# Kernel optimization log

Measured on AMD Instinct MI355X. Metric: run time of the kernel, lower is better.

## Reference

```python
import jax, jax.numpy as jnp
import numpy as np
import math

B, S, DIM = 2, 2048, 1024
N_HEADS, N_KV = 16, 4
HD = DIM // N_HEADS          # 64
N_REP = N_HEADS // N_KV      # 4
ROPE_THETA = 5000.0


def _rope_tables(seqlen, head_dim, theta):
    freqs = 1.0 / (theta ** (np.arange(0, head_dim, 2, dtype=np.float32) / head_dim))
    angles = np.outer(np.arange(seqlen, dtype=np.float32), freqs)  # [S, HD/2]
    return jnp.asarray(np.cos(angles)), jnp.asarray(np.sin(angles))


def setup_inputs() -> dict:
    key = jax.random.key(0)
    ks = jax.random.split(key, 6)
    x = jax.random.normal(ks[0], (B, S, DIM), dtype=jnp.float32)
    cos, sin = _rope_tables(S, HD, ROPE_THETA)
    # additive causal mask: 0 on/below diagonal, -inf above
    mask = jnp.where(jnp.tril(jnp.ones((S, S), dtype=bool)), 0.0, -jnp.inf).astype(jnp.float32)
    wq = jax.random.normal(ks[1], (DIM, N_HEADS * HD), dtype=jnp.float32) * 0.02
    wk = jax.random.normal(ks[2], (DIM, N_KV * HD), dtype=jnp.float32) * 0.02
    wv = jax.random.normal(ks[3], (DIM, N_KV * HD), dtype=jnp.float32) * 0.02
    wo = jax.random.normal(ks[4], (N_HEADS * HD, DIM), dtype=jnp.float32) * 0.02
    return {"x": x, "cos": cos, "sin": sin, "mask": mask,
            "wq": wq, "wk": wk, "wv": wv, "wo": wo}


def _apply_rope(t, cos, sin):
    # t: [B, S, H, HD]; even/odd interleaved pairs form complex numbers
    te, to = t[..., 0::2], t[..., 1::2]               # [B,S,H,HD/2]
    c = cos[None, :, None, :]
    s = sin[None, :, None, :]
    re = te * c - to * s
    im = te * s + to * c
    return jnp.stack([re, im], axis=-1).reshape(t.shape)  # re-interleave


def reference(x, cos, sin, mask, wq, wk, wv, wo):
    bsz, seqlen, _ = x.shape
    q = (x @ wq).reshape(bsz, seqlen, N_HEADS, HD)
    k = (x @ wk).reshape(bsz, seqlen, N_KV, HD)
    v = (x @ wv).reshape(bsz, seqlen, N_KV, HD)
    q = _apply_rope(q, cos, sin)
    k = _apply_rope(k, cos, sin)
    # GQA: group query heads as [kv_head g, rep r] instead of repeating K/V
    qg = q.reshape(bsz, seqlen, N_KV, N_REP, HD)
    scores = jnp.einsum('bsgrd,btgd->bgrst', qg, k) / math.sqrt(HD)  # [B,G,R,S,S]
    scores = scores + mask[None, None, None, :, :]
    p = jax.nn.softmax(scores, axis=-1)
    out = jnp.einsum('bgrst,btgd->bsgrd', p, v)       # [B,S,G,R,HD]
    out = out.reshape(bsz, seqlen, N_HEADS * HD)
    return out @ wo
```

## Files before the change

### kernel.cpp

```cpp
#include <hip/hip_runtime.h>
#include <math.h>

#define S_LEN 2048
#define B_SZ 2

typedef __bf16 bf16_8 __attribute__((ext_vector_type(8)));
typedef float  f32_4  __attribute__((ext_vector_type(4)));

__device__ __forceinline__ unsigned short ftob(float f) {
  union { __bf16 h; unsigned short u; } cv;
  cv.h = (__bf16)f;
  return cv.u;
}

__device__ __forceinline__ void gll16(const unsigned short* g, unsigned short* l) {
  __builtin_amdgcn_global_load_lds(
      (const __attribute__((address_space(1))) unsigned int*)g,
      (__attribute__((address_space(3))) unsigned int*)l, 16, 0, 0);
}

#define QSCALE (0.125f * 1.44269504f)

__device__ __forceinline__ void tr_tile(const float* __restrict__ W,
                                        unsigned short* __restrict__ Wt,
                                        int N, int bx, int by, float (*T)[33])
{
  const int k0 = by * 32, n0 = bx * 32;
  const int r = threadIdx.x >> 3, c4 = (threadIdx.x & 7) * 4;
  const float4 v = *(const float4*)&W[(size_t)(k0 + r) * N + n0 + c4];
  T[r][c4 + 0] = v.x; T[r][c4 + 1] = v.y;
  T[r][c4 + 2] = v.z; T[r][c4 + 3] = v.w;
  __syncthreads();
  ushort4 o;
  o.x = ftob(T[c4 + 0][r]); o.y = ftob(T[c4 + 1][r]);
  o.z = ftob(T[c4 + 2][r]); o.w = ftob(T[c4 + 3][r]);
  *(ushort4*)&Wt[(size_t)(n0 + r) * 1024 + k0 + c4] = o;
}

__global__ __launch_bounds__(256) void prep1(
    const float* __restrict__ x, const float* __restrict__ wq,
    const float* __restrict__ wk, const float* __restrict__ wv,
    unsigned short* __restrict__ xb, unsigned short* __restrict__ wqkvt)
{
  __shared__ float T[32][33];
  const int idx = blockIdx.x;
  if (idx < 1024) {
    tr_tile(wq, wqkvt, 1024, idx & 31, idx >> 5, T);
  } else if (idx < 1280) {
    const int i = idx - 1024;
    tr_tile(wk, wqkvt + 1024 * 1024, 256, i & 7, i >> 3, T);
  } else if (idx < 1536) {
    const int i = idx - 1280;
    tr_tile(wv, wqkvt + 1280 * 1024, 256, i & 7, i >> 3, T);
  } else {
    const int i = idx - 1536;
#pragma unroll
    for (int j = 0; j < 4; ++j) {
      const int id = i * 1024 + (int)threadIdx.x + j * 256;
      const float4 v = ((const float4*)x)[id];
      ushort4 o;
      o.x = ftob(v.x); o.y = ftob(v.y); o.z = ftob(v.z); o.w = ftob(v.w);
      ((ushort4*)xb)[id] = o;
    }
  }
}

__global__ __launch_bounds__(256) void prep2(
    const float* __restrict__ wo, unsigned short* __restrict__ wot)
{
  __shared__ float T[32][33];
  tr_tile(wo, wot, 1024, blockIdx.x & 31, blockIdx.x >> 5, T);
}

__global__ __launch_bounds__(256) void gemm_qkv(
    const unsigned short* __restrict__ A, const unsigned short* __restrict__ Bt,
    unsigned short* __restrict__ qb, unsigned short* __restrict__ Kimg,
    unsigned short* __restrict__ Vimg,
    const float* __restrict__ cosT, const float* __restrict__ sinT)
{
  __shared__ unsigned short sm[9216];
  unsigned short* As = sm;
  unsigned short* Bs = sm + 2048;
  const int bm = blockIdx.y * 64, bn0 = blockIdx.x;
  const int tid = threadIdx.x;
  const int w = tid >> 6, lane = tid & 63, l16 = lane & 15, quad = lane >> 4;
  const int mh = (w & 1) * 32, nh = (w >> 1) * 64;

  f32_4 acc[2][4];
#pragma unroll
  for (int mt = 0; mt < 2; ++mt)
#pragma unroll
    for (int nt = 0; nt < 4; ++nt) acc[mt][nt] = (f32_4){0.f, 0.f, 0.f, 0.f};

  for (int k0 = 0; k0 < 1024; k0 += 32) {
    __syncthreads();
    gll16(&A[(size_t)(bm + (tid >> 2)) * 1024 + k0 + (tid & 3) * 8], &As[tid * 8]);
    gll16(&Bt[(size_t)(bn0 * 128 + (tid >> 2)) * 1024 + k0 + (tid & 3) * 8], &Bs[tid * 8]);
    {
      const int cb = tid + 256;
      gll16(&Bt[(size_t)(bn0 * 128 + (cb >> 2)) * 1024 + k0 + (cb & 3) * 8], &Bs[cb * 8]);
    }
    __syncthreads();
    bf16_8 af[2], bf[4];
#pragma unroll
    for (int mt = 0; mt < 2; ++mt)
      af[mt] = *(const bf16_8*)&As[(mh + mt * 16 + l16) * 32 + quad * 8];
#pragma unroll
    for (int nt = 0; nt < 4; ++nt)
      bf[nt] = *(const bf16_8*)&Bs[(nh + nt * 16 + l16) * 32 + quad * 8];
#pragma unroll
    for (int mt = 0; mt < 2; ++mt)
#pragma unroll
      for (int nt = 0; nt < 4; ++nt)
        acc[mt][nt] = __builtin_amdgcn_mfma_f32_16x16x32_bf16(af[mt], bf[nt], acc[mt][nt], 0, 0, 0);
  }

  const int colbase = bn0 * 128;
  if (colbase < 1024) {
#pragma unroll
    for (int mt = 0; mt < 2; ++mt)
#pragma unroll
      for (int r = 0; r < 4; ++r) {
        const int row = bm + mh + mt * 16 + quad * 4 + r;
        const int s = row & (S_LEN - 1);
#pragma unroll
        for (int nt = 0; nt < 4; ++nt) {
          const int col = colbase + nh + nt * 16 + l16;
          float val = acc[mt][nt][r];
          const float pv = __shfl_xor(val, 1);
          const int fi = (col & 63) >> 1;
          const float cc = cosT[s * 32 + fi], ss = sinT[s * 32 + fi];
          val = (l16 & 1) ? fmaf(pv, ss, val * cc) : fmaf(val, cc, -(pv * ss));
          qb[(size_t)row * 1024 + col] = ftob(val * QSCALE);
        }
      }
  } else if (colbase < 1280) {
#pragma unroll
    for (int mt = 0; mt < 2; ++mt)
#pragma unroll
      for (int r = 0; r < 4; ++r) {
        const int row = bm + mh + mt * 16 + quad * 4 + r;
        const int s = row & (S_LEN - 1), bi = row >> 11;
        const int tile = s >> 6, key = s & 63;
#pragma unroll
        for (int nt = 0; nt < 4; ++nt) {
          const int col = colbase + nh + nt * 16 + l16;
          float val = acc[mt][nt][r];
          const float pv = __shfl_xor(val, 1);
          const int fi = (col & 63) >> 1;
          const float cc = cosT[s * 32 + fi], ss = sinT[s * 32 + fi];
          val = (l16 & 1) ? fmaf(pv, ss, val * cc) : fmaf(val, cc, -(pv * ss));
          const int gcol = col - 1024, g = gcol >> 6, d = gcol & 63;
          Kimg[(size_t)((bi * 4 + g) * 32 + tile) * 4608 + key * 72 + d] = ftob(val);
        }
      }
  } else {
    __syncthreads();
    const int half = nh >> 6;
    unsigned short* Ts = sm + half * 4608;
#pragma unroll
    for (int mt = 0; mt < 2; ++mt)
#pragma unroll
      for (int r = 0; r < 4; ++r) {
        const int key = mh + mt * 16 + quad * 4 + r;
#pragma unroll
        for (int nt = 0; nt < 4; ++nt) {
          const int d = nt * 16 + l16;
          Ts[d * 72 + key] = ftob(acc[mt][nt][r]);
        }
      }
    __syncthreads();
    const int bi = bm >> 11, tile = (bm & 2047) >> 6;
#pragma unroll
    for (int it = 0; it < 4; ++it) {
      const int c = tid + it * 256;
      const int hh = c >> 9, cc = c & 511;
      const int d = cc >> 3, k8 = (cc & 7) * 8;
      const int g = (bn0 - 10) * 2 + hh;
      const uint4 v = *(const uint4*)&sm[hh * 4608 + d * 72 + k8];
      *(uint4*)&Vimg[(size_t)((bi * 4 + g) * 32 + tile) * 4608 + d * 72 + k8] = v;
    }
  }
}

__global__ __launch_bounds__(256) void gemm_wo(
    const unsigned short* __restrict__ A, const unsigned short* __restrict__ Bt,
    float* __restrict__ C)
{
  __shared__ unsigned short sm[6144];
  unsigned short* As = sm;
  unsigned short* Bs = sm + 2048;
  const int bm = blockIdx.y * 64, bn0 = blockIdx.x;
  const int tid = threadIdx.x;
  const int w = tid >> 6, lane = tid & 63, l16 = lane & 15, quad = lane >> 4;
  const int mh = (w & 1) * 32, nh = (w >> 1) * 64;

  f32_4 acc[2][4];
#pragma unroll
  for (int mt = 0; mt < 2; ++mt)
#pragma unroll
    for (int nt = 0; nt < 4; ++nt) acc[mt][nt] = (f32_4){0.f, 0.f, 0.f, 0.f};

  for (int k0 = 0; k0 < 1024; k0 += 32) {
    __syncthreads();
    gll16(&A[(size_t)(bm + (tid >> 2)) * 1024 + k0 + (tid & 3) * 8], &As[tid * 8]);
    gll16(&Bt[(size_t)(bn0 * 128 + (tid >> 2)) * 1024 + k0 + (tid & 3) * 8], &Bs[tid * 8]);
    {
      const int cb = tid + 256;
      gll16(&Bt[(size_t)(bn0 * 128 + (cb >> 2)) * 1024 + k0 + (cb & 3) * 8], &Bs[cb * 8]);
    }
    __syncthreads();
    bf16_8 af[2], bf[4];
#pragma unroll
    for (int mt = 0; mt < 2; ++mt)
      af[mt] = *(const bf16_8*)&As[(mh + mt * 16 + l16) * 32 + quad * 8];
#pragma unroll
    for (int nt = 0; nt < 4; ++nt)
      bf[nt] = *(const bf16_8*)&Bs[(nh + nt * 16 + l16) * 32 + quad * 8];
#pragma unroll
    for (int mt = 0; mt < 2; ++mt)
#pragma unroll
      for (int nt = 0; nt < 4; ++nt)
        acc[mt][nt] = __builtin_amdgcn_mfma_f32_16x16x32_bf16(af[mt], bf[nt], acc[mt][nt], 0, 0, 0);
  }
#pragma unroll
  for (int mt = 0; mt < 2; ++mt)
#pragma unroll
    for (int r = 0; r < 4; ++r) {
      const int row = bm + mh + mt * 16 + quad * 4 + r;
#pragma unroll
      for (int nt = 0; nt < 4; ++nt)
        C[(size_t)row * 1024 + bn0 * 128 + nh + nt * 16 + l16] = acc[mt][nt][r];
    }
}

__global__ __launch_bounds__(256) void flash_attn_mfma(
    const unsigned short* __restrict__ Q, const unsigned short* __restrict__ Kimg,
    const unsigned short* __restrict__ Vimg, unsigned short* __restrict__ O)
{
  __shared__ unsigned short Ks[64 * 72];
  __shared__ unsigned short Vs[64 * 72];
  __shared__ unsigned short Ps[4][16 * 72];
  const int qt = 31 - blockIdx.x, h = blockIdx.y, b = blockIdx.z;
  const int g = h >> 2;
  const int tid = threadIdx.x;
  const int w = tid >> 6, lane = tid & 63, l16 = lane & 15, quad = lane >> 4;
  unsigned short* ps = Ps[w];

  const unsigned short* qp =
      Q + ((size_t)(b * S_LEN + qt * 64 + w * 16 + l16)) * 1024 + h * 64;
  const bf16_8 bq0 = *(const bf16_8*)(qp + quad * 8);
  const bf16_8 bq1 = *(const bf16_8*)(qp + 32 + quad * 8);

  f32_4 o[4];
#pragma unroll
  for (int mt = 0; mt < 4; ++mt) o[mt] = (f32_4){0.f, 0.f, 0.f, 0.f};
  float l_part = 0.f;

  const unsigned short* kim = Kimg + (size_t)((b * 4 + g) * 32) * 4608;
  const unsigned short* vim = Vimg + (size_t)((b * 4 + g) * 32) * 4608;

  for (int tile = 0; tile <= qt; ++tile) {
    __syncthreads();
    const unsigned short* kp = kim + (size_t)tile * 4608;
    const unsigned short* vp = vim + (size_t)tile * 4608;
#pragma unroll
    for (int i = 0; i < 4; ++i) {
      const int c = tid + i * 256;
      if (c < 576) gll16(kp + c * 8, Ks + c * 8);
      else         gll16(vp + (c - 576) * 8, Vs + (c - 576) * 8);
    }
    if (tid < 128) {
      const int c = tid + 1024;
      gll16(vp + (c - 576) * 8, Vs + (c - 576) * 8);
    }
    __syncthreads();

    const bool diag = (tile == qt);
#pragma unroll
    for (int mt = 0; mt < 4; ++mt) {
      f32_4 z = (f32_4){0.f, 0.f, 0.f, 0.f};
      const bf16_8 kf0 = *(const bf16_8*)&Ks[(mt * 16 + l16) * 72 + quad * 8];
      const bf16_8 kf1 = *(const bf16_8*)&Ks[(mt * 16 + l16) * 72 + 32 + quad * 8];
      z = __builtin_amdgcn_mfma_f32_16x16x32_bf16(kf0, bq0, z, 0, 0, 0);
      z = __builtin_amdgcn_mfma_f32_16x16x32_bf16(kf1, bq1, z, 0, 0, 0);
      ushort4 pk;
#pragma unroll
      for (int r = 0; r < 4; ++r) {
        float p = __builtin_amdgcn_exp2f(z[r]);
        if (diag && (mt * 16 + quad * 4 + r > w * 16 + l16)) p = 0.f;
        l_part += p;
        ((unsigned short*)&pk)[r] = ftob(p);
      }
      *(ushort4*)&ps[l16 * 72 + mt * 16 + quad * 4] = pk;
    }
    const bf16_8 pf0 = *(const bf16_8*)&ps[l16 * 72 + quad * 8];
    const bf16_8 pf1 = *(const bf16_8*)&ps[l16 * 72 + 32 + quad * 8];
#pragma unroll
    for (int mt = 0; mt < 4; ++mt) {
      const bf16_8 vf0 = *(const bf16_8*)&Vs[(mt * 16 + l16) * 72 + quad * 8];
      const bf16_8 vf1 = *(const bf16_8*)&Vs[(mt * 16 + l16) * 72 + 32 + quad * 8];
      o[mt] = __builtin_amdgcn_mfma_f32_16x16x32_bf16(vf0, pf0, o[mt], 0, 0, 0);
      o[mt] = __builtin_amdgcn_mfma_f32_16x16x32_bf16(vf1, pf1, o[mt], 0, 0, 0);
    }
  }

  float l = l_part;
  l += __shfl_xor(l, 16);
  l += __shfl_xor(l, 32);
  const float inv = 1.f / l;
  const int qrow = qt * 64 + w * 16 + l16;
  unsigned short* op = O + ((size_t)(b * S_LEN + qrow)) * 1024 + h * 64;
#pragma unroll
  for (int mt = 0; mt < 4; ++mt) {
    ushort4 ov;
#pragma unroll
    for (int r = 0; r < 4; ++r) ((unsigned short*)&ov)[r] = ftob(o[mt][r] * inv);
    *(ushort4*)&op[mt * 16 + quad * 4] = ov;
  }
}

extern "C" void kernel_launch(void* const* d_in, const int* in_sizes, int n_in,
                              void* d_out, int out_size, void* d_ws, size_t ws_size,
                              hipStream_t stream)
{
  const float* x    = (const float*)d_in[0];
  const float* cosT = (const float*)d_in[1];
  const float* sinT = (const float*)d_in[2];
  const float* wq   = (const float*)d_in[4];
  const float* wk   = (const float*)d_in[5];
  const float* wv   = (const float*)d_in[6];
  const float* wo   = (const float*)d_in[7];
  float* out = (float*)d_out;

  char* ws = (char*)d_ws;
  const size_t MB = 1024 * 1024;
  unsigned short* xb    = (unsigned short*)(ws);
  unsigned short* wot   = (unsigned short*)(ws);
  unsigned short* qb    = (unsigned short*)(ws + 8 * MB);
  unsigned short* wqkvt = (unsigned short*)(ws + 16 * MB);
  unsigned short* Kimg  = (unsigned short*)(ws + 19 * MB);
  unsigned short* Vimg  = (unsigned short*)(ws + 19 * MB + 2359296);

  prep1<<<2560, 256, 0, stream>>>(x, wq, wk, wv, xb, wqkvt);
  gemm_qkv<<<dim3(12, 64), 256, 0, stream>>>(xb, wqkvt, qb, Kimg, Vimg, cosT, sinT);
  prep2<<<1024, 256, 0, stream>>>(wo, wot);
  flash_attn_mfma<<<dim3(32, 16, 2), 256, 0, stream>>>(qb, Kimg, Vimg, qb);
  gemm_wo<<<dim3(8, 64), 256, 0, stream>>>(qb, wot, out);
}
```

Baseline: 203.5 us.

## Share K/V tiles across a GQA group and pass P through lane shuffles

The attention kernel now assigns one block per KV group and 32-query chunk, with each of the four waves handling a different query head of that group. Each K/V tile loaded into LDS is therefore reused by four heads instead of one, which cuts global and LDS load traffic. The P fragments are rearranged with cross-lane shuffles instead of being stored to and read back from shared memory. The wo transpose is also folded into the first prep kernel, removing one launch. The trade-offs are more registers per wave, since each wave holds two query fragments, and a smaller grid of 512 blocks, which may lower occupancy.

```diff
diff --git a/kernel.cpp b/kernel.cpp
--- a/kernel.cpp
+++ b/kernel.cpp
@@ -11,6 +11,9 @@
   union { __bf16 h; unsigned short u; } cv;
   cv.h = (__bf16)f;
   return cv.u;
+}
+__device__ __forceinline__ unsigned int pack2(float a, float b) {
+  return (unsigned int)ftob(a) | ((unsigned int)ftob(b) << 16);
 }
 
 __device__ __forceinline__ void gll16(const unsigned short* g, unsigned short* l) {
@@ -37,10 +40,12 @@
   *(ushort4*)&Wt[(size_t)(n0 + r) * 1024 + k0 + c4] = o;
 }
 
-__global__ __launch_bounds__(256) void prep1(
+__global__ __launch_bounds__(256) void prep(
     const float* __restrict__ x, const float* __restrict__ wq,
     const float* __restrict__ wk, const float* __restrict__ wv,
-    unsigned short* __restrict__ xb, unsigned short* __restrict__ wqkvt)
+    const float* __restrict__ wo,
+    unsigned short* __restrict__ xb, unsigned short* __restrict__ wqkvt,
+    unsigned short* __restrict__ wot)
 {
   __shared__ float T[32][33];
   const int idx = blockIdx.x;
@@ -52,8 +57,11 @@
   } else if (idx < 1536) {
     const int i = idx - 1280;
     tr_tile(wv, wqkvt + 1280 * 1024, 256, i & 7, i >> 3, T);
+  } else if (idx < 2560) {
+    const int i = idx - 1536;
+    tr_tile(wo, wot, 1024, i & 31, i >> 5, T);
   } else {
-    const int i = idx - 1536;
+    const int i = idx - 2560;
 #pragma unroll
     for (int j = 0; j < 4; ++j) {
       const int id = i * 1024 + (int)threadIdx.x + j * 256;
@@ -63,13 +71,6 @@
       ((ushort4*)xb)[id] = o;
     }
   }
-}
-
-__global__ __launch_bounds__(256) void prep2(
-    const float* __restrict__ wo, unsigned short* __restrict__ wot)
-{
-  __shared__ float T[32][33];
-  tr_tile(wo, wot, 1024, blockIdx.x & 31, blockIdx.x >> 5, T);
 }
 
 __global__ __launch_bounds__(256) void gemm_qkv(
@@ -234,33 +235,40 @@
     }
 }
 
-__global__ __launch_bounds__(256) void flash_attn_mfma(
+__global__ __launch_bounds__(256) void flash_attn_v3(
     const unsigned short* __restrict__ Q, const unsigned short* __restrict__ Kimg,
     const unsigned short* __restrict__ Vimg, unsigned short* __restrict__ O)
 {
   __shared__ unsigned short Ks[64 * 72];
   __shared__ unsigned short Vs[64 * 72];
-  __shared__ unsigned short Ps[4][16 * 72];
-  const int qt = 31 - blockIdx.x, h = blockIdx.y, b = blockIdx.z;
-  const int g = h >> 2;
+  const int qc = 63 - blockIdx.x;
+  const int g = blockIdx.y, b = blockIdx.z;
   const int tid = threadIdx.x;
   const int w = tid >> 6, lane = tid & 63, l16 = lane & 15, quad = lane >> 4;
-  unsigned short* ps = Ps[w];
-
-  const unsigned short* qp =
-      Q + ((size_t)(b * S_LEN + qt * 64 + w * 16 + l16)) * 1024 + h * 64;
-  const bf16_8 bq0 = *(const bf16_8*)(qp + quad * 8);
-  const bf16_8 bq1 = *(const bf16_8*)(qp + 32 + quad * 8);
-
-  f32_4 o[4];
-#pragma unroll
-  for (int mt = 0; mt < 4; ++mt) o[mt] = (f32_4){0.f, 0.f, 0.f, 0.f};
-  float l_part = 0.f;
+  const int h = g * 4 + w;
+  const int qbase = qc * 32;
+
+  bf16_8 bq[2][2];
+#pragma unroll
+  for (int qf = 0; qf < 2; ++qf) {
+    const unsigned short* qp =
+        Q + ((size_t)(b * S_LEN + qbase + qf * 16 + l16)) * 1024 + h * 64;
+    bq[qf][0] = *(const bf16_8*)(qp + quad * 8);
+    bq[qf][1] = *(const bf16_8*)(qp + 32 + quad * 8);
+  }
+
+  f32_4 acc[2][4];
+#pragma unroll
+  for (int qf = 0; qf < 2; ++qf)
+#pragma unroll
+    for (int mt = 0; mt < 4; ++mt) acc[qf][mt] = (f32_4){0.f, 0.f, 0.f, 0.f};
+  float l_part[2] = {0.f, 0.f};
 
   const unsigned short* kim = Kimg + (size_t)((b * 4 + g) * 32) * 4608;
   const unsigned short* vim = Vimg + (size_t)((b * 4 + g) * 32) * 4608;
-
-  for (int tile = 0; tile <= qt; ++tile) {
+  const int ntiles = (qc >> 1) + 1;
+
+  for (int tile = 0; tile < ntiles; ++tile) {
     __syncthreads();
     const unsigned short* kp = kim + (size_t)tile * 4608;
     const unsigned short* vp = vim + (size_t)tile * 4608;
@@ -276,47 +284,83 @@
     }
     __syncthreads();
 
-    const bool diag = (tile == qt);
+    const bool diag = (tile == ntiles - 1);
+    unsigned int pk[2][4][2];
 #pragma unroll
     for (int mt = 0; mt < 4; ++mt) {
-      f32_4 z = (f32_4){0.f, 0.f, 0.f, 0.f};
       const bf16_8 kf0 = *(const bf16_8*)&Ks[(mt * 16 + l16) * 72 + quad * 8];
       const bf16_8 kf1 = *(const bf16_8*)&Ks[(mt * 16 + l16) * 72 + 32 + quad * 8];
-      z = __builtin_amdgcn_mfma_f32_16x16x32_bf16(kf0, bq0, z, 0, 0, 0);
-      z = __builtin_amdgcn_mfma_f32_16x16x32_bf16(kf1, bq1, z, 0, 0, 0);
-      ushort4 pk;
-#pragma unroll
-      for (int r = 0; r < 4; ++r) {
-        float p = __builtin_amdgcn_exp2f(z[r]);
-        if (diag && (mt * 16 + quad * 4 + r > w * 16 + l16)) p = 0.f;
-        l_part += p;
-        ((unsigned short*)&pk)[r] = ftob(p);
-      }
-      *(ushort4*)&ps[l16 * 72 + mt * 16 + quad * 4] = pk;
-    }
-    const bf16_8 pf0 = *(const bf16_8*)&ps[l16 * 72 + quad * 8];
-    const bf16_8 pf1 = *(const bf16_8*)&ps[l16 * 72 + 32 + quad * 8];
+#pragma unroll
+      for (int qf = 0; qf < 2; ++qf) {
+        f32_4 z = (f32_4){0.f, 0.f, 0.f, 0.f};
+        z = __builtin_amdgcn_mfma_f32_16x16x32_bf16(kf0, bq[qf][0], z, 0, 0, 0);
+        z = __builtin_amdgcn_mfma_f32_16x16x32_bf16(kf1, bq[qf][1], z, 0, 0, 0);
+        float p[4];
+#pragma unroll
+        for (int r = 0; r < 4; ++r) {
+          float pv = __builtin_amdgcn_exp2f(z[r]);
+          if (diag) {
+            const int keyl = mt * 16 + quad * 4 + r;
+            const int ql = (qc & 1) * 32 + qf * 16 + l16;
+            pv = (keyl > ql) ? 0.f : pv;
+          }
+          l_part[qf] += pv;
+          p[r] = pv;
+        }
+        pk[qf][mt][0] = pack2(p[0], p[1]);
+        pk[qf][mt][1] = pack2(p[2], p[3]);
+      }
+    }
+    const int srcA = (quad & 1) * 32 + l16;
+    const int srcB = srcA + 16;
+    const bool hiq = (quad >> 1) != 0;
+    bf16_8 pfrag[2][2];
+#pragma unroll
+    for (int qf = 0; qf < 2; ++qf)
+#pragma unroll
+      for (int H = 0; H < 2; ++H) {
+        const unsigned int lo0 = __shfl((int)pk[qf][2 * H][0], srcA);
+        const unsigned int lo1 = __shfl((int)pk[qf][2 * H][1], srcA);
+        const unsigned int lo2 = __shfl((int)pk[qf][2 * H][0], srcB);
+        const unsigned int lo3 = __shfl((int)pk[qf][2 * H][1], srcB);
+        const unsigned int hi0 = __shfl((int)pk[qf][2 * H + 1][0], srcA);
+        const unsigned int hi1 = __shfl((int)pk[qf][2 * H + 1][1], srcA);
+        const unsigned int hi2 = __shfl((int)pk[qf][2 * H + 1][0], srcB);
+        const unsigned int hi3 = __shfl((int)pk[qf][2 * H + 1][1], srcB);
+        uint4 u;
+        u.x = hiq ? hi0 : lo0;
+        u.y = hiq ? hi1 : lo1;
+        u.z = hiq ? hi2 : lo2;
+        u.w = hiq ? hi3 : lo3;
+        pfrag[qf][H] = *(const bf16_8*)&u;
+      }
 #pragma unroll
     for (int mt = 0; mt < 4; ++mt) {
       const bf16_8 vf0 = *(const bf16_8*)&Vs[(mt * 16 + l16) * 72 + quad * 8];
       const bf16_8 vf1 = *(const bf16_8*)&Vs[(mt * 16 + l16) * 72 + 32 + quad * 8];
-      o[mt] = __builtin_amdgcn_mfma_f32_16x16x32_bf16(vf0, pf0, o[mt], 0, 0, 0);
-      o[mt] = __builtin_amdgcn_mfma_f32_16x16x32_bf16(vf1, pf1, o[mt], 0, 0, 0);
-    }
-  }
-
-  float l = l_part;
-  l += __shfl_xor(l, 16);
-  l += __shfl_xor(l, 32);
-  const float inv = 1.f / l;
-  const int qrow = qt * 64 + w * 16 + l16;
-  unsigned short* op = O + ((size_t)(b * S_LEN + qrow)) * 1024 + h * 64;
-#pragma unroll
-  for (int mt = 0; mt < 4; ++mt) {
-    ushort4 ov;
-#pragma unroll
-    for (int r = 0; r < 4; ++r) ((unsigned short*)&ov)[r] = ftob(o[mt][r] * inv);
-    *(ushort4*)&op[mt * 16 + quad * 4] = ov;
+#pragma unroll
+      for (int qf = 0; qf < 2; ++qf) {
+        acc[qf][mt] = __builtin_amdgcn_mfma_f32_16x16x32_bf16(vf0, pfrag[qf][0], acc[qf][mt], 0, 0, 0);
+        acc[qf][mt] = __builtin_amdgcn_mfma_f32_16x16x32_bf16(vf1, pfrag[qf][1], acc[qf][mt], 0, 0, 0);
+      }
+    }
+  }
+
+#pragma unroll
+  for (int qf = 0; qf < 2; ++qf) {
+    float l = l_part[qf];
+    l += __shfl_xor(l, 16);
+    l += __shfl_xor(l, 32);
+    const float inv = 1.f / l;
+    unsigned short* op =
+        O + ((size_t)(b * S_LEN + qbase + qf * 16 + l16)) * 1024 + h * 64;
+#pragma unroll
+    for (int mt = 0; mt < 4; ++mt) {
+      ushort4 ov;
+#pragma unroll
+      for (int r = 0; r < 4; ++r) ((unsigned short*)&ov)[r] = ftob(acc[qf][mt][r] * inv);
+      *(ushort4*)&op[mt * 16 + quad * 4] = ov;
+    }
   }
 }
 
@@ -336,15 +380,14 @@
   char* ws = (char*)d_ws;
   const size_t MB = 1024 * 1024;
   unsigned short* xb    = (unsigned short*)(ws);
-  unsigned short* wot   = (unsigned short*)(ws);
   unsigned short* qb    = (unsigned short*)(ws + 8 * MB);
   unsigned short* wqkvt = (unsigned short*)(ws + 16 * MB);
   unsigned short* Kimg  = (unsigned short*)(ws + 19 * MB);
   unsigned short* Vimg  = (unsigned short*)(ws + 19 * MB + 2359296);
-
-  prep1<<<2560, 256, 0, stream>>>(x, wq, wk, wv, xb, wqkvt);
+  unsigned short* wot   = (unsigned short*)(ws + 24641536);
+
+  prep<<<3584, 256, 0, stream>>>(x, wq, wk, wv, wo, xb, wqkvt, wot);
   gemm_qkv<<<dim3(12, 64), 256, 0, stream>>>(xb, wqkvt, qb, Kimg, Vimg, cosT, sinT);
-  prep2<<<1024, 256, 0, stream>>>(wo, wot);
-  flash_attn_mfma<<<dim3(32, 16, 2), 256, 0, stream>>>(qb, Kimg, Vimg, qb);
+  flash_attn_v3<<<dim3(64, 4, 2), 256, 0, stream>>>(qb, Kimg, Vimg, qb);
   gemm_wo<<<dim3(8, 64), 256, 0, stream>>>(qb, wot, out);
 }
```

Measured after the change: 206.3 us. No clear change (+1.4%).
